# Performance work log

Measured on AMD Instinct MI355X. Metric: run time of the kernel, lower is better.

Reference implementation:

```python
import jax, jax.numpy as jnp
import numpy as np
from jax import lax

ROUTINGS = 3
SCALING = 2
NUM_CAPSULE = 8
NUM_ATOMS = 16
EPS = 1e-9


def squash(v):
    # SegCaps squash: v * |v|^2 / ((1+|v|^2) * |v|), norm over last axis
    sq = jnp.sum(v * v, axis=-1, keepdims=True)
    return v * sq / ((1.0 + sq) * jnp.sqrt(sq + EPS))


def setup_inputs() -> dict:
    key = jax.random.key(0)
    k1, k2 = jax.random.split(key)
    B, H, Wd, Cin, Ain = 4, 56, 56, 8, 32
    x = jax.random.normal(k1, (B, H, Wd, Cin, Ain), dtype=jnp.float32)
    # TF conv2d_transpose filter layout: [k, k, out_ch, in_ch]
    W = jax.random.normal(k2, (4, 4, NUM_CAPSULE * NUM_ATOMS, Ain), dtype=jnp.float32) * 0.05
    b = 0.1 * jnp.ones((1, 1, NUM_CAPSULE, NUM_ATOMS), dtype=jnp.float32)
    return {"x": x, "W": W, "b": b}


def reference(x, W, b):
    B, H, Wd, Cin, Ain = x.shape
    Cout, Aout = NUM_CAPSULE, NUM_ATOMS
    # [B,H,W,Cin,A] -> [Cin,B,H,W,A] -> [Cin*B,H,W,A]  (faithful to original ordering)
    xt = jnp.transpose(x, (3, 0, 1, 2, 4)).reshape(Cin * B, H, Wd, Ain)
    # TF conv2d_transpose, SAME padding, stride=scaling: out spatial = in * scaling
    out = lax.conv_transpose(
        xt, W, strides=(SCALING, SCALING), padding="SAME",
        dimension_numbers=("NHWC", "HWIO", "NHWC"), transpose_kernel=True)
    Hp, Wp = out.shape[1], out.shape[2]
    # votes: [B, Cin, Hp, Wp, Cout, Aout]  (faithful to original reshape)
    votes = out.reshape(B, Cin, Hp, Wp, Cout, Aout)
    biases = jnp.broadcast_to(b, (Hp, Wp, Cout, Aout))
    logits = jnp.zeros((B, Cin, Hp, Wp, Cout), dtype=x.dtype)
    act = None
    for i in range(ROUTINGS):
        route = jax.nn.softmax(logits, axis=-1)                      # [B,Cin,Hp,Wp,Cout]
        pre = jnp.einsum("bihwc,bihwca->bhwca", route, votes) + biases
        act = squash(pre)                                            # [B,Hp,Wp,Cout,Aout]
        if i < ROUTINGS - 1:
            logits = logits + jnp.einsum("bihwca,bhwca->bihwc", votes, act)
    return act
```

## Files before the change

kernel.cpp:

```cpp
#include <hip/hip_runtime.h>
#include <math.h>

#define CEPS 1e-9f

typedef _Float16 half8 __attribute__((ext_vector_type(8)));
typedef float floatx16 __attribute__((ext_vector_type(16)));


template<int CTRL>
__device__ __forceinline__ float dpp_add(float v) {
    return v + __int_as_float(__builtin_amdgcn_update_dpp(
        0, __float_as_int(v), CTRL, 0xF, 0xF, false));
}

__device__ __forceinline__ float sum_i8(float v) {
    v = dpp_add<0xB1>(v);
    v = dpp_add<0x4E>(v);
    v = dpp_add<0x141>(v);
    return v;
}

__device__ __forceinline__ float4 sel4(bool c, float4 a, float4 b) {
    return make_float4(c ? a.x : b.x, c ? a.y : b.y, c ? a.z : b.z, c ? a.w : b.w);
}

__global__ __launch_bounds__(256) void prep_w(const float* __restrict__ Wt,
                                              _Float16* __restrict__ wb) {
    int idx = blockIdx.x * 256 + threadIdx.x;
    int parity = idx >> 11;
    int s = (idx >> 8) & 7;
    int t = (idx >> 6) & 3;
    int l = idx & 63;
    int rh = parity >> 1, rw = parity & 1;
    int n = t * 32 + (l & 31);
    int h = l >> 5;
    int ci0 = ((s & 1) << 4) + (h << 3);
    int kh = ((s >> 2) << 1) + 1 - rh;
    int kw = (((s >> 1) & 1) << 1) + 1 - rw;
    const float* src = Wt + (((kh * 4 + kw) * 128 + n) << 5) + ci0;
    float4 w0 = *(const float4*)src;
    float4 w1 = *(const float4*)(src + 4);
    half8 hv;
    hv[0] = (_Float16)w0.x; hv[1] = (_Float16)w0.y;
    hv[2] = (_Float16)w0.z; hv[3] = (_Float16)w0.w;
    hv[4] = (_Float16)w1.x; hv[5] = (_Float16)w1.y;
    hv[6] = (_Float16)w1.z; hv[7] = (_Float16)w1.w;
    *(half8*)(wb + ((long)idx << 3)) = hv;
}

__global__ __launch_bounds__(256, 3) void caps_mfma(
    const float* __restrict__ x,
    const _Float16* __restrict__ wb,
    const float* __restrict__ bias,
    float* __restrict__ out)
{
    __shared__ _Float16 xt[25 * 8 * 40];
    __shared__ float scx[4][1152];

    const int tid = threadIdx.x;
    const int tile = blockIdx.x;
    const int tu = tile / 14, tv = tile - tu * 14;
    const int u0 = tu * 4, v0 = tv * 4;
    const int rh = blockIdx.y >> 1;
    const int rw = blockIdx.y & 1;
    const int bp = blockIdx.z;
    const _Float16* wsrc = wb + ((long)blockIdx.y << 14);

    #pragma unroll
    for (int it = 0; it < 4; ++it) {
        int idx = tid + (it << 8);
        if (idx < 800) {
            int cell = idx >> 5;
            int r = idx & 31;
            int i = r >> 2;
            int ci0 = (r & 3) << 3;
            int ri = cell / 5, rj = cell - ri * 5;
            int gi = u0 + rh - 1 + ri;
            int gj = v0 + rw - 1 + rj;
            float tmp[8] = {0.f, 0.f, 0.f, 0.f, 0.f, 0.f, 0.f, 0.f};
            if ((unsigned)gi < 56u && (unsigned)gj < 56u) {
                const float* src = x + (((i & 3) * 56 + gi) * 56 + gj) * 256
                                     + ((bp * 2 + (i >> 2)) << 5) + ci0;
                float4 a0 = *(const float4*)src;
                float4 a1 = *(const float4*)(src + 4);
                tmp[0] = a0.x; tmp[1] = a0.y; tmp[2] = a0.z; tmp[3] = a0.w;
                tmp[4] = a1.x; tmp[5] = a1.y; tmp[6] = a1.z; tmp[7] = a1.w;
            }
            half8 hv;
            #pragma unroll
            for (int j = 0; j < 8; ++j) hv[j] = (_Float16)tmp[j];
            *(half8*)(xt + (cell * 8 + i) * 40 + ci0) = hv;
        }
    }
    __syncthreads();

    const int l = tid & 63;
    const int w = tid >> 6;
    const int col = l & 31, h = l >> 5;
    const int invA = (l & 31) * 40 + (h << 3);

    floatx16 acc[4];
    #pragma unroll
    for (int t = 0; t < 4; ++t)
        #pragma unroll
        for (int j = 0; j < 16; ++j) acc[t][j] = 0.f;

    #pragma unroll
    for (int s = 0; s < 8; ++s) {
        const int tkh = s >> 2;
        const int tkw = (s >> 1) & 1;
        const int row = w + 1 - tkh;
        const int aoff = (row * 5 + 1 - tkw) * 320 + ((s & 1) << 4) + invA;
        half8 af = *(const half8*)(xt + aoff);
        #pragma unroll
        for (int t = 0; t < 4; ++t) {
            half8 bf = *(const half8*)(wsrc + (((s * 4 + t) * 64 + l) << 3));
            acc[t] = __builtin_amdgcn_mfma_f32_32x32x16_f16(af, bf, acc[t], 0, 0, 0);
        }
    }

    float* scb = &scx[w][0];
    const int cI = l >> 3;
    const int iI = l & 7;

    float4 bq[4];
    #pragma unroll
    for (int t = 0; t < 4; ++t) bq[t] = *(const float4*)(bias + cI * 16 + t * 4);

    #pragma unroll
    for (int pixl = 0; pixl < 4; ++pixl) {
        #pragma unroll
        for (int t = 0; t < 4; ++t)
            #pragma unroll
            for (int il = 0; il < 4; ++il)
                scb[(t * 32 + col) * 9 + (h << 2) + il] = acc[t][pixl * 4 + il];
        float va[16];
        #pragma unroll
        for (int a = 0; a < 16; ++a) va[a] = scb[(cI * 16 + a) * 9 + iI];

        float pre[16], lg = 0.f;

        #pragma unroll
        for (int a = 0; a < 16; ++a) {
            float s = sum_i8(va[a]);
            pre[a] = fmaf(0.125f, s, (&bq[a >> 2].x)[a & 3]);
        }
        {
            float nq = pre[0] * pre[0];
            #pragma unroll
            for (int a = 1; a < 16; ++a) nq = fmaf(pre[a], pre[a], nq);
            float sc = nq * __builtin_amdgcn_rcpf(1.f + nq)
                          * __builtin_amdgcn_rsqf(nq + CEPS);
            #pragma unroll
            for (int a = 0; a < 16; ++a) pre[a] *= sc;
            float d = va[0] * pre[0];
            #pragma unroll
            for (int a = 1; a < 16; ++a) d = fmaf(va[a], pre[a], d);
            lg = d;
        }

        #pragma unroll
        for (int r = 1; r < 3; ++r) {
            float e = __expf(lg);
            float ss = dpp_add<0x128>(e);
            ss += __shfl_xor(ss, 16);
            ss += __shfl_xor(ss, 32);
            float route = e * __builtin_amdgcn_rcpf(ss);
            #pragma unroll
            for (int a = 0; a < 16; ++a) {
                float m = sum_i8(route * va[a]);
                pre[a] = m + (&bq[a >> 2].x)[a & 3];
            }
            float nq = pre[0] * pre[0];
            #pragma unroll
            for (int a = 1; a < 16; ++a) nq = fmaf(pre[a], pre[a], nq);
            float sc = nq * __builtin_amdgcn_rcpf(1.f + nq)
                          * __builtin_amdgcn_rsqf(nq + CEPS);
            #pragma unroll
            for (int a = 0; a < 16; ++a) pre[a] *= sc;
            if (r < 2) {
                float d = va[0] * pre[0];
                #pragma unroll
                for (int a = 1; a < 16; ++a) d = fmaf(va[a], pre[a], d);
                lg += d;
            }
        }

        float4 q0 = make_float4(pre[0],  pre[1],  pre[2],  pre[3]);
        float4 q1 = make_float4(pre[4],  pre[5],  pre[6],  pre[7]);
        float4 q2 = make_float4(pre[8],  pre[9],  pre[10], pre[11]);
        float4 q3 = make_float4(pre[12], pre[13], pre[14], pre[15]);
        float4 t0 = sel4((iI & 1) != 0, q1, q0);
        float4 t1 = sel4((iI & 1) != 0, q3, q2);
        float4 o4 = sel4((iI & 2) != 0, t1, t0);
        if (iI < 4) {
            const int p = ((u0 + w) << 1) + rh;
            const int q = ((v0 + pixl) << 1) + rw;
            *(float4*)(out + (((bp * 112 + p) * 112 + q) << 7) + cI * 16 + iI * 4) = o4;
        }
    }
}

extern "C" void kernel_launch(void* const* d_in, const int* in_sizes, int n_in,
                              void* d_out, int out_size, void* d_ws, size_t ws_size,
                              hipStream_t stream) {
    const float* x  = (const float*)d_in[0];
    const float* Wt = (const float*)d_in[1];
    const float* b  = (const float*)d_in[2];
    float* out = (float*)d_out;
    _Float16* wb = (_Float16*)d_ws;

    prep_w<<<32, 256, 0, stream>>>(Wt, wb);
    dim3 grid(196, 4, 4);
    caps_mfma<<<grid, 256, 0, stream>>>(x, wb, b, out);
}
```

Before: 122.3 us.

## Switch to 16x16x32 MFMA with 4x2 pixel tiles and more blocks

Replaces the 32x32x16 MFMA tiling (4x4 pixel tiles, 16-wide accumulators) with 16x16x32 MFMA over 4x2 pixel tiles. Weight prep is relaid out to match, the input staging in shared memory shrinks to a 3x5 halo, and the grid doubles. Accumulator registers per thread drop, which allows occupancy hint 4. The cost is more halo reloads per output and a branchy scatter of accumulators into shared memory per pixel.

```diff
diff --git a/kernel.cpp b/kernel.cpp
--- a/kernel.cpp
+++ b/kernel.cpp
@@ -4,7 +4,7 @@
 #define CEPS 1e-9f
 
 typedef _Float16 half8 __attribute__((ext_vector_type(8)));
-typedef float floatx16 __attribute__((ext_vector_type(16)));
+typedef float floatx4 __attribute__((ext_vector_type(4)));
 
 
 template<int CTRL>
@@ -28,15 +28,14 @@
                                               _Float16* __restrict__ wb) {
     int idx = blockIdx.x * 256 + threadIdx.x;
     int parity = idx >> 11;
-    int s = (idx >> 8) & 7;
-    int t = (idx >> 6) & 3;
+    int s = (idx >> 9) & 3;
+    int t = (idx >> 6) & 7;
     int l = idx & 63;
     int rh = parity >> 1, rw = parity & 1;
-    int n = t * 32 + (l & 31);
-    int h = l >> 5;
-    int ci0 = ((s & 1) << 4) + (h << 3);
-    int kh = ((s >> 2) << 1) + 1 - rh;
-    int kw = (((s >> 1) & 1) << 1) + 1 - rw;
+    int n = t * 16 + (l & 15);
+    int ci0 = (l >> 4) << 3;
+    int kh = ((s >> 1) << 1) + 1 - rh;
+    int kw = ((s & 1) << 1) + 1 - rw;
     const float* src = Wt + (((kh * 4 + kw) * 128 + n) << 5) + ci0;
     float4 w0 = *(const float4*)src;
     float4 w1 = *(const float4*)(src + 4);
@@ -48,33 +47,33 @@
     *(half8*)(wb + ((long)idx << 3)) = hv;
 }
 
-__global__ __launch_bounds__(256, 3) void caps_mfma(
+__global__ __launch_bounds__(256, 4) void caps_mfma(
     const float* __restrict__ x,
     const _Float16* __restrict__ wb,
     const float* __restrict__ bias,
     float* __restrict__ out)
 {
-    __shared__ _Float16 xt[25 * 8 * 40];
+    __shared__ _Float16 xt[15 * 8 * 40];
     __shared__ float scx[4][1152];
 
     const int tid = threadIdx.x;
     const int tile = blockIdx.x;
-    const int tu = tile / 14, tv = tile - tu * 14;
-    const int u0 = tu * 4, v0 = tv * 4;
+    const int tu = tile / 28, tv = tile - tu * 28;
+    const int u0 = tu * 4, v0 = tv * 2;
     const int rh = blockIdx.y >> 1;
     const int rw = blockIdx.y & 1;
     const int bp = blockIdx.z;
     const _Float16* wsrc = wb + ((long)blockIdx.y << 14);
 
     #pragma unroll
-    for (int it = 0; it < 4; ++it) {
+    for (int it = 0; it < 2; ++it) {
         int idx = tid + (it << 8);
-        if (idx < 800) {
+        if (idx < 480) {
             int cell = idx >> 5;
             int r = idx & 31;
             int i = r >> 2;
             int ci0 = (r & 3) << 3;
-            int ri = cell / 5, rj = cell - ri * 5;
+            int ri = cell / 3, rj = cell - ri * 3;
             int gi = u0 + rh - 1 + ri;
             int gj = v0 + rw - 1 + rj;
             float tmp[8] = {0.f, 0.f, 0.f, 0.f, 0.f, 0.f, 0.f, 0.f};
@@ -96,44 +95,48 @@
 
     const int l = tid & 63;
     const int w = tid >> 6;
-    const int col = l & 31, h = l >> 5;
-    const int invA = (l & 31) * 40 + (h << 3);
-
-    floatx16 acc[4];
-    #pragma unroll
-    for (int t = 0; t < 4; ++t)
-        #pragma unroll
-        for (int j = 0; j < 16; ++j) acc[t][j] = 0.f;
-
-    #pragma unroll
-    for (int s = 0; s < 8; ++s) {
-        const int tkh = s >> 2;
-        const int tkw = (s >> 1) & 1;
-        const int row = w + 1 - tkh;
-        const int aoff = (row * 5 + 1 - tkw) * 320 + ((s & 1) << 4) + invA;
-        half8 af = *(const half8*)(xt + aoff);
-        #pragma unroll
-        for (int t = 0; t < 4; ++t) {
-            half8 bf = *(const half8*)(wsrc + (((s * 4 + t) * 64 + l) << 3));
-            acc[t] = __builtin_amdgcn_mfma_f32_32x32x16_f16(af, bf, acc[t], 0, 0, 0);
+    const int q = l >> 4;
+    const int pixA = (l & 15) >> 3;
+    const int iA = l & 7;
+
+    floatx4 acc[8];
+    #pragma unroll
+    for (int t = 0; t < 8; ++t)
+        #pragma unroll
+        for (int j = 0; j < 4; ++j) acc[t][j] = 0.f;
+
+    #pragma unroll
+    for (int s = 0; s < 4; ++s) {
+        const int tkh = s >> 1, tkw = s & 1;
+        const int ucell = w + 1 - tkh;
+        const int vcell = pixA + 1 - tkw;
+        half8 af = *(const half8*)(xt + ((ucell * 3 + vcell) * 8 + iA) * 40 + (q << 3));
+        #pragma unroll
+        for (int t = 0; t < 8; ++t) {
+            half8 bf = *(const half8*)(wsrc + (((s * 8 + t) * 64 + l) << 3));
+            acc[t] = __builtin_amdgcn_mfma_f32_16x16x32_f16(af, bf, acc[t], 0, 0, 0);
         }
     }
 
     float* scb = &scx[w][0];
     const int cI = l >> 3;
     const int iI = l & 7;
+    const int myPix = l >> 5;
+    const int iRow = ((l >> 4) & 1) << 2;
 
     float4 bq[4];
     #pragma unroll
     for (int t = 0; t < 4; ++t) bq[t] = *(const float4*)(bias + cI * 16 + t * 4);
 
     #pragma unroll
-    for (int pixl = 0; pixl < 4; ++pixl) {
-        #pragma unroll
-        for (int t = 0; t < 4; ++t)
-            #pragma unroll
-            for (int il = 0; il < 4; ++il)
-                scb[(t * 32 + col) * 9 + (h << 2) + il] = acc[t][pixl * 4 + il];
+    for (int pixl = 0; pixl < 2; ++pixl) {
+        if (myPix == pixl) {
+            #pragma unroll
+            for (int t = 0; t < 8; ++t)
+                #pragma unroll
+                for (int reg = 0; reg < 4; ++reg)
+                    scb[(t * 16 + (l & 15)) * 9 + iRow + reg] = acc[t][reg];
+        }
         float va[16];
         #pragma unroll
         for (int a = 0; a < 16; ++a) va[a] = scb[(cI * 16 + a) * 9 + iI];
@@ -195,8 +198,8 @@
         float4 o4 = sel4((iI & 2) != 0, t1, t0);
         if (iI < 4) {
             const int p = ((u0 + w) << 1) + rh;
-            const int q = ((v0 + pixl) << 1) + rw;
-            *(float4*)(out + (((bp * 112 + p) * 112 + q) << 7) + cI * 16 + iI * 4) = o4;
+            const int qq = ((v0 + pixl) << 1) + rw;
+            *(float4*)(out + (((bp * 112 + p) * 112 + qq) << 7) + cI * 16 + iI * 4) = o4;
         }
     }
 }
@@ -211,6 +214,6 @@
     _Float16* wb = (_Float16*)d_ws;
 
     prep_w<<<32, 256, 0, stream>>>(Wt, wb);
-    dim3 grid(196, 4, 4);
+    dim3 grid(392, 4, 4);
     caps_mfma<<<grid, 256, 0, stream>>>(x, wb, b, out);
 }
```

New measurement: 131.9 us. 1.08x slower.
